# Optimization experiments

Measured on AMD Instinct MI355X. Metric: run time of the kernel, lower is better.

The kernel has to match this reference:

```python
import jax, jax.numpy as jnp
import numpy as np

PAD_IND = 3
SOS_IND = 0
NSTEPS = 25
H = 256   # hidden_size
D = 256   # input_size (embedding dim)
L = 3     # lstm_layers


def _lstm_cell(x, h, c, Wih, Whh, bih, bhh):
    # torch LSTM gate order: i, f, g, o
    g = x @ Wih.T + bih + h @ Whh.T + bhh
    i, f, gg, o = jnp.split(g, 4, axis=-1)
    c2 = jax.nn.sigmoid(f) * c + jax.nn.sigmoid(i) * jnp.tanh(gg)
    h2 = jax.nn.sigmoid(o) * jnp.tanh(c2)
    return h2, c2


def setup_inputs() -> dict:
    key = jax.random.key(0)
    ks = jax.random.split(key, 24)
    B, T = 64, 256
    Vin, C = 32000, 32000
    s = 1.0 / np.sqrt(H)

    def u(k, shape):
        return jax.random.uniform(k, shape, jnp.float32, -s, s)

    return dict(
        x=jax.random.randint(ks[0], (B, T), 0, Vin),
        target_val=jax.random.randint(ks[1], (B, NSTEPS), 0, C),
        enc_embed=jax.random.normal(ks[2], (Vin, D), jnp.float32),
        enc_Wih=u(ks[3], (L, 4 * H, D)),
        enc_Whh=u(ks[4], (L, 4 * H, H)),
        enc_bih=u(ks[5], (L, 4 * H)),
        enc_bhh=u(ks[6], (L, 4 * H)),
        Wq=u(ks[7], (H, H)), bq=u(ks[8], (H,)),
        Wk=u(ks[9], (H, H)), bk=u(ks[10], (H,)),
        Wv=u(ks[11], (H, H)), bv=u(ks[12], (H,)),
        Wo=u(ks[13], (H, H)), bo=u(ks[14], (H,)),
        dec_embed=jax.random.normal(ks[15], (C, D), jnp.float32),
        dec_Wih0=u(ks[16], (4 * H, 2 * H)),            # decoder layer 0 input is [emb; ctx] = 2H
        dec_Wih_rest=u(ks[17], (L - 1, 4 * H, H)),
        dec_Whh=u(ks[18], (L, 4 * H, H)),
        dec_bih=u(ks[19], (L, 4 * H)),
        dec_bhh=u(ks[20], (L, 4 * H)),
        dec_W=u(ks[21], (C, H)),
        dec_b=u(ks[22], (C,)),
    )


def reference(x, target_val, enc_embed, enc_Wih, enc_Whh, enc_bih, enc_bhh,
              Wq, bq, Wk, bk, Wv, bv, Wo, bo,
              dec_embed, dec_Wih0, dec_Wih_rest, dec_Whh, dec_bih, dec_bhh,
              dec_W, dec_b):
    B, T = x.shape
    lengths = (x != PAD_IND).sum(axis=1)            # [B], emulates pack_padded_sequence
    emb = enc_embed[x]                              # [B,T,D]
    valid = (jnp.arange(T)[:, None] < lengths[None, :])[..., None]  # [T,B,1]
    h0 = jnp.zeros((L, B, H), emb.dtype)
    c0 = jnp.zeros((L, B, H), emb.dtype)

    def enc_step(carry, inp):
        h, c = carry
        xt, v = inp
        hs, cs = [], []
        z = xt
        for l in range(L):
            hl, cl = _lstm_cell(z, h[l], c[l], enc_Wih[l], enc_Whh[l], enc_bih[l], enc_bhh[l])
            hl = jnp.where(v, hl, h[l])             # freeze state past sequence length
            cl = jnp.where(v, cl, c[l])
            hs.append(hl); cs.append(cl)
            z = hl
        h = jnp.stack(hs); c = jnp.stack(cs)
        return (h, c), jnp.where(v, h[-1], 0.0)     # pad_packed pads with zeros

    (enc_h, enc_c), outs = jax.lax.scan(enc_step, (h0, c0), (jnp.swapaxes(emb, 0, 1), valid))
    enc_hiddens = jnp.swapaxes(outs, 0, 1)          # [B,T,H]

    # attention key/value projections are loop-invariant -> hoist out of decode loop
    kp = enc_hiddens @ Wk.T + bk                    # [B,T,H]
    vp = enc_hiddens @ Wv.T + bv                    # [B,T,H]
    scale = 1.0 / jnp.sqrt(jnp.asarray(H, emb.dtype))
    dec_Wih = [dec_Wih0, dec_Wih_rest[0], dec_Wih_rest[1]]
    tok0 = jnp.full((B,), SOS_IND, jnp.int32)

    def dec_step(carry, _):
        h, c, tok = carry
        e = dec_embed[tok]                          # [B,D]
        q = h.sum(axis=0) @ Wq.T + bq               # prev_state[0].sum(axis=0) -> [B,H]
        scores = jnp.einsum('bh,bth->bt', q, kp) * scale
        attn = jax.nn.softmax(scores, axis=-1)
        ctx = jnp.einsum('bt,bth->bh', attn, vp) @ Wo.T + bo
        z = jnp.concatenate([e, ctx], axis=-1)      # [B,2H]
        hs, cs = [], []
        for l in range(L):
            hl, cl = _lstm_cell(z, h[l], c[l], dec_Wih[l], dec_Whh[l], dec_bih[l], dec_bhh[l])
            hs.append(hl); cs.append(cl)
            z = hl
        h = jnp.stack(hs); c = jnp.stack(cs)
        logits = z @ dec_W.T + dec_b                # [B,C]
        tok = jnp.argmax(logits, axis=-1).astype(jnp.int32)  # greedy feedback (TF ratio = 0)
        return (h, c, tok), logits

    _, logits = jax.lax.scan(dec_step, (enc_h, enc_c, tok0), None, length=NSTEPS)  # [25,B,C]
    return jnp.swapaxes(logits, 0, 1)[:, :, None, :]  # [B,25,1,C] like the torch module
```

## Files before the change

kernel.cpp:

```cpp
#include <hip/hip_runtime.h>
#include <math.h>

#define TT    256
#define NB    64
#define HH    256
#define NSTEP 25
#define NCLS  32000
#define PADI  3
#define RING  4

__device__ __align__(16) float g_hring[3][RING][NB][HH];
__device__ __align__(16) float g_enchid[TT][NB][HH];
__device__ __align__(16) float g_kp[NB][TT][HH];
__device__ __align__(16) float g_vp[NB][TT][HH];
__device__ __align__(16) float g_cfin[3][NB][HH];
__device__ __align__(16) float g_hdec[2][3][NB][HH];
__device__ __align__(16) float g_z0[NB][512];
__device__ float    g_wmax[256][NB];
__device__ int      g_wmaxi[256][NB];
__device__ int      g_len[NB];
__device__ unsigned g_arrive[256];
__device__ unsigned g_rel[256];
__device__ unsigned g_earr[3][64];
__device__ unsigned g_erel[3][64];

__device__ __forceinline__ float sigf(float v){ return 1.0f / (1.0f + expf(-v)); }

#define SCOPE_AG __HIP_MEMORY_SCOPE_AGENT
typedef unsigned long long u64;
__device__ __forceinline__ float2 ld2(const float* p){
  u64 v = __hip_atomic_load((const u64*)p, __ATOMIC_RELAXED, SCOPE_AG);
  float2 r; __builtin_memcpy(&r, &v, 8); return r;
}
__device__ __forceinline__ float ldc(const float* p){ return __hip_atomic_load(p, __ATOMIC_RELAXED, SCOPE_AG); }
__device__ __forceinline__ void  stc(float* p, float v){ __hip_atomic_store(p, v, __ATOMIC_RELAXED, SCOPE_AG); }
__device__ __forceinline__ int   ldi(const int* p){ return __hip_atomic_load(p, __ATOMIC_RELAXED, SCOPE_AG); }
__device__ __forceinline__ void  sti(int* p, int v){ __hip_atomic_store(p, v, __ATOMIC_RELAXED, SCOPE_AG); }
__device__ __forceinline__ unsigned ldu(const unsigned* p){ return __hip_atomic_load(p, __ATOMIC_RELAXED, SCOPE_AG); }
__device__ __forceinline__ void  stu(unsigned* p, unsigned v){ __hip_atomic_store(p, v, __ATOMIC_RELAXED, SCOPE_AG); }

#define DOT4(a_, x_, w_) (a_) += (x_).x*(w_).x + (x_).y*(w_).y + (x_).z*(w_).z + (x_).w*(w_).w

__global__ void __launch_bounds__(256) k_init(const int* __restrict__ p_x){
  const int blk = blockIdx.x, tid = threadIdx.x;
  if (blk < 192){
    int idx = blk*256 + tid;
    int l = idx >> 14, rem = idx & 16383;
    g_hring[l][RING-1][rem >> 8][rem & 255] = 0.f;
  } else {
    __shared__ int s_c[4];
    int b = blk - 192;
    int cnt = (p_x[b*TT + tid] != PADI) ? 1 : 0;
    #pragma unroll
    for (int m = 1; m < 64; m <<= 1) cnt += __shfl_xor(cnt, m);
    if ((tid & 63) == 0) s_c[tid >> 6] = cnt;
    __syncthreads();
    if (tid == 0) g_len[b] = s_c[0] + s_c[1] + s_c[2] + s_c[3];
  }
  if (blk == 0){ g_arrive[tid] = 0u; g_rel[tid] = 0u; }
  if (blk == 1 && tid < 192){
    ((unsigned*)g_earr)[tid] = 0u;
    ((unsigned*)g_erel)[tid] = 0u;
  }
}

__global__ void __launch_bounds__(512, 1)
k_enc(const int*   __restrict__ p_x,
      const float* __restrict__ p_eemb,
      const float* __restrict__ p_eWih, const float* __restrict__ p_eWhh,
      const float* __restrict__ p_ebih, const float* __restrict__ p_ebhh)
{
  __shared__ __align__(16) float s_W[8192];
  __shared__ float s_gat[1024];
  __shared__ float s_b[16];
  __shared__ int   s_len[64];

  const int w = blockIdx.x, tid = threadIdx.x;
  const int l = w >> 6, q = w & 63;
  const int b2 = tid >> 4, j = tid & 15;
  const int ce = tid >> 6, cb = tid & 63;

  for (int fi = tid; fi < 8192; fi += 512){
    int row = fi >> 9, k = fi & 511;
    int e = row >> 2, g = row & 3;
    int wrow = g*256 + 4*q + e;
    s_W[fi] = (k < 256) ? p_eWih[((size_t)l*1024 + wrow)*256 + k]
                        : p_eWhh[((size_t)l*1024 + wrow)*256 + (k - 256)];
  }
  if (tid < 16){
    int e = tid >> 2, g = tid & 3;
    int wrow = g*256 + 4*q + e;
    s_b[tid] = p_ebih[l*1024 + wrow] + p_ebhh[l*1024 + wrow];
  }
  if (tid < 64) s_len[tid] = g_len[tid];
  float c_reg = 0.f, h_frz = 0.f;
  __syncthreads();

  for (int t = 0; t < TT; ++t){
    if (tid == 0){
      const int li = (q & 3) << 4;
      for (;;){
        bool ok = (ldu(&g_erel[l][li]) >= (unsigned)t);
        if (ok && l > 0)          ok = (ldu(&g_erel[l-1][li]) >= (unsigned)(t+1));
        if (ok && l < 2 && t >= 4) ok = (ldu(&g_erel[l+1][li]) >= (unsigned)(t-3));
        if (ok) break;
        __builtin_amdgcn_s_sleep(1);
      }
    }
    __syncthreads();

    float4 xin[2][4], hin[2][4];
    #pragma unroll
    for (int bb = 0; bb < 2; ++bb){
      const int batch = 2*b2 + bb;
      if (l == 0){
        const float* xs = p_eemb + (size_t)p_x[batch*TT + t]*HH;
        #pragma unroll
        for (int u = 0; u < 4; ++u) xin[bb][u] = *(const float4*)(xs + u*64 + 4*j);
      } else {
        const float* xs = &g_hring[l-1][t & (RING-1)][batch][0];
        #pragma unroll
        for (int u = 0; u < 4; ++u){
          float2 a = ld2(xs + u*64 + 4*j), c = ld2(xs + u*64 + 4*j + 2);
          xin[bb][u] = make_float4(a.x, a.y, c.x, c.y);
        }
      }
      const float* hs = &g_hring[l][(t + RING - 1) & (RING-1)][batch][0];
      #pragma unroll
      for (int u = 0; u < 4; ++u){
        float2 a = ld2(hs + u*64 + 4*j), c = ld2(hs + u*64 + 4*j + 2);
        hin[bb][u] = make_float4(a.x, a.y, c.x, c.y);
      }
    }

    float acc[16][2];
    #pragma unroll
    for (int r = 0; r < 16; ++r){ acc[r][0] = 0.f; acc[r][1] = 0.f; }
    #pragma unroll
    for (int u = 0; u < 8; ++u){
      float4 i0 = (u < 4) ? xin[0][u] : hin[0][u-4];
      float4 i1 = (u < 4) ? xin[1][u] : hin[1][u-4];
      #pragma unroll
      for (int row = 0; row < 16; ++row){
        float4 wv = *(const float4*)&s_W[row*512 + u*64 + 4*j];
        DOT4(acc[row][0], i0, wv);
        DOT4(acc[row][1], i1, wv);
      }
    }
    #pragma unroll
    for (int row = 0; row < 16; ++row){
      #pragma unroll
      for (int bb = 0; bb < 2; ++bb){
        float v = acc[row][bb];
        v += __shfl_xor(v, 1); v += __shfl_xor(v, 2);
        v += __shfl_xor(v, 4); v += __shfl_xor(v, 8);
        acc[row][bb] = v;
      }
    }
    if (j == 0){
      #pragma unroll
      for (int row = 0; row < 16; ++row){
        s_gat[row*64 + 2*b2    ] = acc[row][0];
        s_gat[row*64 + 2*b2 + 1] = acc[row][1];
      }
    }
    __syncthreads();

    if (tid < 256){
      float iv = s_gat[(ce*4+0)*64 + cb] + s_b[ce*4+0];
      float fv = s_gat[(ce*4+1)*64 + cb] + s_b[ce*4+1];
      float gv = s_gat[(ce*4+2)*64 + cb] + s_b[ce*4+2];
      float ov = s_gat[(ce*4+3)*64 + cb] + s_b[ce*4+3];
      float c2 = sigf(fv)*c_reg + sigf(iv)*tanhf(gv);
      float h2 = sigf(ov)*tanhf(c2);
      bool valid = (t < s_len[cb]);
      if (valid) c_reg = c2;
      h_frz = valid ? h2 : h_frz;
      stc(&g_hring[l][t & (RING-1)][cb][4*q + ce], h_frz);
      if (l == 2) g_enchid[t][cb][4*q + ce] = valid ? h_frz : 0.f;
    }

    asm volatile("s_waitcnt vmcnt(0)" ::: "memory");
    __syncthreads();
    if (tid == 0) stu(&g_earr[l][q], (unsigned)(t+1));
    if (q == 0 && tid < 64){
      while (!__all(ldu(&g_earr[l][tid]) >= (unsigned)(t+1)))
        __builtin_amdgcn_s_sleep(1);
      if (tid < 4) stu(&g_erel[l][tid << 4], (unsigned)(t+1));
    }
    __syncthreads();
  }

  if (tid < 256) g_cfin[l][cb][4*q + ce] = c_reg;
}

__device__ __forceinline__ void gbar(int w, unsigned target){
  asm volatile("s_waitcnt vmcnt(0)" ::: "memory");
  __syncthreads();
  if (threadIdx.x == 0) stu(&g_arrive[w], target);
  if (w == 0){
    if (threadIdx.x < 64){
      const int i4 = threadIdx.x * 4;
      for (;;){
        unsigned a0 = ldu(&g_arrive[i4+0]);
        unsigned a1 = ldu(&g_arrive[i4+1]);
        unsigned a2 = ldu(&g_arrive[i4+2]);
        unsigned a3 = ldu(&g_arrive[i4+3]);
        if (__all((a0>=target) && (a1>=target) && (a2>=target) && (a3>=target))) break;
        __builtin_amdgcn_s_sleep(1);
      }
      if (threadIdx.x < 16) stu(&g_rel[threadIdx.x << 4], target);
    }
  } else {
    if (threadIdx.x == 0){
      const unsigned* line = &g_rel[(w >> 4) << 4];
      while (ldu(line) < target) __builtin_amdgcn_s_sleep(1);
    }
  }
  __syncthreads();
}

template<int NCB, int BASE>
__device__ __forceinline__ void dec_gates(const float* sw, const float* i0, const float* i1,
                                          const float* i2, int j, float out4[4]){
  float a0=0.f, a1=0.f, a2=0.f, a3=0.f;
  const float* ips[3] = { i0, i1, i2 };
  #pragma unroll
  for (int cb = 0; cb < NCB; ++cb){
    float2 xin[16];
    #pragma unroll
    for (int u = 0; u < 16; ++u) xin[u] = ld2(ips[cb] + u*16 + 2*j);
    #pragma unroll
    for (int u2 = 0; u2 < 8; ++u2){
      float2 pa = xin[2*u2], pb = xin[2*u2+1];
      const float* wb = &sw[BASE + (((cb*4+0)*8+j)*36) + u2*4];
      float4 w0 = *(const float4*)(wb);
      float4 w1 = *(const float4*)(wb + 288);
      float4 w2 = *(const float4*)(wb + 576);
      float4 w3 = *(const float4*)(wb + 864);
      a0 += pa.x*w0.x + pa.y*w0.y + pb.x*w0.z + pb.y*w0.w;
      a1 += pa.x*w1.x + pa.y*w1.y + pb.x*w1.z + pb.y*w1.w;
      a2 += pa.x*w2.x + pa.y*w2.y + pb.x*w2.z + pb.y*w2.w;
      a3 += pa.x*w3.x + pa.y*w3.y + pb.x*w3.z + pb.y*w3.w;
    }
  }
  #pragma unroll
  for (int m = 1; m < 8; m <<= 1){
    a0 += __shfl_xor(a0, m); a1 += __shfl_xor(a1, m);
    a2 += __shfl_xor(a2, m); a3 += __shfl_xor(a3, m);
  }
  out4[0]=a0; out4[1]=a1; out4[2]=a2; out4[3]=a3;
}

__global__ void __launch_bounds__(512, 1)
k_dec(const float* __restrict__ p_Wq, const float* __restrict__ p_bq,
      const float* __restrict__ p_Wk, const float* __restrict__ p_bk,
      const float* __restrict__ p_Wv, const float* __restrict__ p_bv,
      const float* __restrict__ p_Wo, const float* __restrict__ p_bo,
      const float* __restrict__ p_demb,
      const float* __restrict__ p_dWih0, const float* __restrict__ p_dWihR,
      const float* __restrict__ p_dWhh,
      const float* __restrict__ p_dbih,  const float* __restrict__ p_dbhh,
      const float* __restrict__ p_dW,    const float* __restrict__ p_db,
      float* __restrict__ p_out)
{
  __shared__ __align__(16) float s_w[8064];
  __shared__ __align__(16) float s_h2[NB*HH];
  __shared__ float s_bdec[12];
  __shared__ __align__(16) float s_hs[256];
  __shared__ __align__(16) float s_q[256];
  __shared__ __align__(16) float s_sc[256];
  __shared__ __align__(16) float s_at[256];
  __shared__ __align__(16) float s_ctx[256];
  __shared__ float s_rv[8];  __shared__ int s_ri[8];

  const int w   = blockIdx.x;
  const int tid = threadIdx.x;
  const int b   = tid >> 3;
  const int j   = tid & 7;
  unsigned bar  = 0;

  {
    const int b3 = w >> 2, t0 = (w & 3) * 64;
    const int n1 = tid & 127, rq = tid >> 7;
    for (int p = 0; p < 4; ++p){
      const int n = p*128 + n1;
      const float* wrow = (n < 256) ? (p_Wk + (size_t)n*HH) : (p_Wv + (size_t)(n-256)*HH);
      const float bias  = (n < 256) ? p_bk[n] : p_bv[n-256];
      const float4* wr4 = (const float4*)wrow;
      const float* hb = &g_enchid[t0 + rq*16][b3][0];
      const float4* hr[16];
      #pragma unroll
      for (int r = 0; r < 16; ++r) hr[r] = (const float4*)(hb + (size_t)r*NB*HH);
      float a16[16];
      #pragma unroll
      for (int r = 0; r < 16; ++r) a16[r] = 0.f;
      for (int k4 = 0; k4 < 64; ++k4){
        float4 wv = wr4[k4];
        #pragma unroll
        for (int r = 0; r < 16; ++r){ float4 h4 = hr[r][k4]; DOT4(a16[r], h4, wv); }
      }
      float* orow = (n < 256) ? &g_kp[b3][t0 + rq*16][n] : &g_vp[b3][t0 + rq*16][n-256];
      #pragma unroll
      for (int r = 0; r < 16; ++r) stc(orow + (size_t)r*HH, a16[r] + bias);
    }
  }

  for (int fi = tid; fi < 3072; fi += 512){
    int g = fi / 768, k = fi % 768; int row = g*256 + w;
    float v = (k < 512) ? p_dWih0[(size_t)row*512 + k]
                        : p_dWhh[(size_t)row*HH + (k - 512)];
    int cb = k >> 8, kk = k & 255;
    s_w[(((cb*4 + g)*8 + ((kk & 15) >> 1))*36) + (((kk >> 4) << 1) | (kk & 1))] = v;
  }
  for (int fi = tid; fi < 2048; fi += 512){
    int g = fi / 512, k = fi % 512; int row = g*256 + w;
    float v = (k < 256) ? p_dWihR[(size_t)row*HH + k]
                        : p_dWhh[(size_t)(1024 + row)*HH + (k - 256)];
    int cb = k >> 8, kk = k & 255;
    s_w[3456 + (((cb*4 + g)*8 + ((kk & 15) >> 1))*36) + (((kk >> 4) << 1) | (kk & 1))] = v;
  }
  for (int fi = tid; fi < 2048; fi += 512){
    int g = fi / 512, k = fi % 512; int row = g*256 + w;
    float v = (k < 256) ? p_dWihR[(size_t)(1024 + row)*HH + k]
                        : p_dWhh[(size_t)(2048 + row)*HH + (k - 256)];
    int cb = k >> 8, kk = k & 255;
    s_w[5760 + (((cb*4 + g)*8 + ((kk & 15) >> 1))*36) + (((kk >> 4) << 1) | (kk & 1))] = v;
  }
  if (tid < 12){
    int l = tid >> 2, g = tid & 3; int row = g*256 + w;
    s_bdec[tid] = p_dbih[l*1024 + row] + p_dbhh[l*1024 + row];
  }
  gbar(w, ++bar);

  if (tid < 192){
    int fi = w*192 + tid;
    int l = fi >> 14, rem = fi & 16383;
    stc(&g_hdec[0][l][rem >> 8][rem & 255], ldc(&g_hring[l][RING-1][rem >> 8][rem & 255]));
  }
  float c_d0 = 0.f, c_d1 = 0.f, c_d2 = 0.f;
  if (j == 0){
    c_d0 = g_cfin[0][b][w]; c_d1 = g_cfin[1][b][w]; c_d2 = g_cfin[2][b][w];
  }
  gbar(w, ++bar);

  for (int st = 0; st < NSTEP; ++st){
    const int slot = st & 1, nxt = slot ^ 1;

    if (w < 64){
      const int bA = w;
      int tok = 0;
      if (st > 0){
        float v = -1e38f; int idx = 0;
        if (tid < 256){ v = ldc(&g_wmax[tid][bA]); idx = ldi(&g_wmaxi[tid][bA]); }
        #pragma unroll
        for (int m = 1; m < 64; m <<= 1){
          float ov = __shfl_xor(v, m); int oi = __shfl_xor(idx, m);
          if (ov > v || (ov == v && oi < idx)){ v = ov; idx = oi; }
        }
        if ((tid & 63) == 0){ s_rv[tid >> 6] = v; s_ri[tid >> 6] = idx; }
        __syncthreads();
        if (tid == 0){
          float bv2 = s_rv[0]; int bi2 = s_ri[0];
          for (int q2 = 1; q2 < 8; ++q2){
            float ov = s_rv[q2]; int oi = s_ri[q2];
            if (ov > bv2 || (ov == bv2 && oi < bi2)){ bv2 = ov; bi2 = oi; }
          }
          s_ri[0] = bi2;
        }
        __syncthreads();
        tok = s_ri[0];
      }
      if (tid < 256)
        s_hs[tid] = ldc(&g_hdec[slot][0][bA][tid]) + ldc(&g_hdec[slot][1][bA][tid])
                  + ldc(&g_hdec[slot][2][bA][tid]);
      __syncthreads();
      if (tid < 256){
        float a = p_bq[tid];
        const float4* wr = (const float4*)(p_Wq + (size_t)tid*HH);
        #pragma unroll 8
        for (int k4 = 0; k4 < 64; ++k4){
          float4 wv = wr[k4]; float4 h4 = *(const float4*)&s_hs[k4*4]; DOT4(a, h4, wv);
        }
        s_q[tid] = a;
      }
      __syncthreads();
      if (tid < 256){
        float a = 0.f;
        const float4* kr = (const float4*)&g_kp[bA][tid][0];
        #pragma unroll 8
        for (int k4 = 0; k4 < 64; ++k4){
          float4 kv = kr[k4]; float4 q4 = *(const float4*)&s_q[k4*4]; DOT4(a, q4, kv);
        }
        s_sc[tid] = a * 0.0625f;
      }
      __syncthreads();
      {
        float sv = (tid < 256) ? s_sc[tid] : -1e38f;
        float m2 = sv;
        #pragma unroll
        for (int m = 1; m < 64; m <<= 1) m2 = fmaxf(m2, __shfl_xor(m2, m));
        if ((tid & 63) == 0) s_rv[tid >> 6] = m2;
        __syncthreads();
        if (tid == 0){ float mm = s_rv[0]; for (int q2 = 1; q2 < 8; ++q2) mm = fmaxf(mm, s_rv[q2]); s_rv[0] = mm; }
        __syncthreads();
        const float mx = s_rv[0];
        float ev = (tid < 256) ? expf(sv - mx) : 0.f;
        float ss = ev;
        #pragma unroll
        for (int m = 1; m < 64; m <<= 1) ss += __shfl_xor(ss, m);
        __syncthreads();
        if ((tid & 63) == 0) s_rv[tid >> 6] = ss;
        __syncthreads();
        if (tid == 0){ float t2 = 0.f; for (int q2 = 0; q2 < 8; ++q2) t2 += s_rv[q2]; s_rv[0] = t2; }
        __syncthreads();
        if (tid < 256) s_at[tid] = ev / s_rv[0];
      }
      __syncthreads();
      if (tid < 256){
        float a = 0.f;
        const float* vb = &g_vp[bA][0][tid];
        #pragma unroll 4
        for (int t4 = 0; t4 < 64; ++t4){
          float4 a4 = *(const float4*)&s_at[t4*4];
          a += a4.x*vb[(size_t)(t4*4+0)*HH] + a4.y*vb[(size_t)(t4*4+1)*HH]
             + a4.z*vb[(size_t)(t4*4+2)*HH] + a4.w*vb[(size_t)(t4*4+3)*HH];
        }
        s_ctx[tid] = a;
      }
      __syncthreads();
      if (tid < 256){
        float a = p_bo[tid];
        const float4* wr = (const float4*)(p_Wo + (size_t)tid*HH);
        #pragma unroll 8
        for (int k4 = 0; k4 < 64; ++k4){
          float4 wv = wr[k4]; float4 c4 = *(const float4*)&s_ctx[k4*4]; DOT4(a, c4, wv);
        }
        stc(&g_z0[bA][256 + tid], a);
        stc(&g_z0[bA][tid], p_demb[(size_t)tok*HH + tid]);
      }
    }
    gbar(w, ++bar);

    {
      float g4[4];
      dec_gates<3, 0>(s_w, &g_z0[b][0], &g_z0[b][256], &g_hdec[slot][0][b][0], j, g4);
      if (j == 0){
        float iv = g4[0]+s_bdec[0], fv = g4[1]+s_bdec[1], gv = g4[2]+s_bdec[2], ov = g4[3]+s_bdec[3];
        float c2 = sigf(fv)*c_d0 + sigf(iv)*tanhf(gv); c_d0 = c2;
        stc(&g_hdec[nxt][0][b][w], sigf(ov)*tanhf(c2));
      }
    }
    gbar(w, ++bar);
    {
      float g4[4];
      dec_gates<2, 3456>(s_w, &g_hdec[nxt][0][b][0], &g_hdec[slot][1][b][0], nullptr, j, g4);
      if (j == 0){
        float iv = g4[0]+s_bdec[4], fv = g4[1]+s_bdec[5], gv = g4[2]+s_bdec[6], ov = g4[3]+s_bdec[7];
        float c2 = sigf(fv)*c_d1 + sigf(iv)*tanhf(gv); c_d1 = c2;
        stc(&g_hdec[nxt][1][b][w], sigf(ov)*tanhf(c2));
      }
    }
    gbar(w, ++bar);
    {
      float g4[4];
      dec_gates<2, 5760>(s_w, &g_hdec[nxt][1][b][0], &g_hdec[slot][2][b][0], nullptr, j, g4);
      if (j == 0){
        float iv = g4[0]+s_bdec[8], fv = g4[1]+s_bdec[9], gv = g4[2]+s_bdec[10], ov = g4[3]+s_bdec[11];
        float c2 = sigf(fv)*c_d2 + sigf(iv)*tanhf(gv); c_d2 = c2;
        stc(&g_hdec[nxt][2][b][w], sigf(ov)*tanhf(c2));
      }
    }
    gbar(w, ++bar);

    {
      {
        const float* src = &g_hdec[nxt][2][0][0];
        #pragma unroll
        for (int u = 0; u < 16; ++u){
          int fo = 2*(tid + 512*u);
          float2 v = ld2(src + fo);
          *(float2*)(s_h2 + fo) = v;
        }
      }
      __syncthreads();

      const int cs = tid & 63, qb = tid >> 6;
      const bool ok0 = (2*cs)   < 125;
      const bool ok1 = (2*cs+1) < 125;
      const int c0 = w*125 + 2*cs, c1 = c0 + 1;
      const float4* wr0 = (const float4*)(p_dW + (size_t)(ok0 ? c0 : w*125)*HH);
      const float4* wr1 = (const float4*)(p_dW + (size_t)(ok1 ? c1 : w*125)*HH);
      const float4* zr[8];
      #pragma unroll
      for (int r = 0; r < 8; ++r) zr[r] = (const float4*)&s_h2[(qb*8 + r)*HH];
      float a0[8], a1[8];
      #pragma unroll
      for (int r = 0; r < 8; ++r){ a0[r] = 0.f; a1[r] = 0.f; }
      for (int k4 = 0; k4 < 64; ++k4){
        float4 w0 = wr0[k4], w1 = wr1[k4];
        #pragma unroll
        for (int r = 0; r < 8; ++r){
          float4 z4 = zr[r][k4];
          DOT4(a0[r], z4, w0);
          DOT4(a1[r], z4, w1);
        }
      }
      const float bias0 = ok0 ? p_db[c0] : 0.f;
      const float bias1 = ok1 ? p_db[c1] : 0.f;
      #pragma unroll
      for (int r = 0; r < 8; ++r){
        const int bb = qb*8 + r;
        float val0 = a0[r] + bias0, val1 = a1[r] + bias1;
        float* orow = p_out + ((size_t)bb*NSTEP + st)*NCLS;
        if (ok0) orow[c0] = val0;
        if (ok1) orow[c1] = val1;
        float v = ok0 ? val0 : -1e38f;
        int idx  = ok0 ? c0 : 0x7fffffff;
        if (ok1 && val1 > v){ v = val1; idx = c1; }
        #pragma unroll
        for (int m = 1; m < 64; m <<= 1){
          float ov = __shfl_xor(v, m); int oi = __shfl_xor(idx, m);
          if (ov > v || (ov == v && oi < idx)){ v = ov; idx = oi; }
        }
        if (cs == 0){ stc(&g_wmax[w][bb], v); sti(&g_wmaxi[w][bb], idx); }
      }
    }
    gbar(w, ++bar);
  }
}

extern "C" void kernel_launch(void* const* d_in, const int* in_sizes, int n_in,
                              void* d_out, int out_size, void* d_ws, size_t ws_size,
                              hipStream_t stream){
  (void)in_sizes; (void)n_in; (void)out_size; (void)d_ws; (void)ws_size;
  const int*   x     = (const int*)d_in[0];
  const float* eemb  = (const float*)d_in[2];
  const float* eWih  = (const float*)d_in[3];
  const float* eWhh  = (const float*)d_in[4];
  const float* ebih  = (const float*)d_in[5];
  const float* ebhh  = (const float*)d_in[6];
  const float* Wq    = (const float*)d_in[7];
  const float* bq    = (const float*)d_in[8];
  const float* Wk    = (const float*)d_in[9];
  const float* bk    = (const float*)d_in[10];
  const float* Wv    = (const float*)d_in[11];
  const float* bv    = (const float*)d_in[12];
  const float* Wo    = (const float*)d_in[13];
  const float* bo    = (const float*)d_in[14];
  const float* demb  = (const float*)d_in[15];
  const float* dWih0 = (const float*)d_in[16];
  const float* dWihR = (const float*)d_in[17];
  const float* dWhh  = (const float*)d_in[18];
  const float* dbih  = (const float*)d_in[19];
  const float* dbhh  = (const float*)d_in[20];
  const float* dW    = (const float*)d_in[21];
  const float* db    = (const float*)d_in[22];
  float* out = (float*)d_out;

  k_init<<<dim3(256), dim3(256), 0, stream>>>(x);
  k_enc<<<dim3(192), dim3(512), 0, stream>>>(x, eemb, eWih, eWhh, ebih, ebhh);
  k_dec<<<dim3(256), dim3(512), 0, stream>>>(Wq, bq, Wk, bk, Wv, bv, Wo, bo,
                                             demb, dWih0, dWihR, dWhh, dbih, dbhh,
                                             dW, db, out);
}
```

Measured before the change: 5.717 ms.

## Split persistent decoder into per-step kernel launches and retile encoder dot products

Replaces the persistent decoder kernel and its software grid barriers with a sequence of small kernels per decode step (attention, three LSTM layers, output projection), using kernel boundaries as synchronization and keeping cell state in global memory. The encoder matvec is also retiled so each thread group covers 4 batches with 32-lane reductions instead of 2 batches with 16-lane reductions. This removes spin-barrier overhead but adds about 125 kernel launches plus reloading decoder weights into shared memory every step.

After: 7.895 ms. +38.1%, slower.

```diff
diff --git a/kernel.cpp b/kernel.cpp
--- a/kernel.cpp
+++ b/kernel.cpp
@@ -15,12 +15,11 @@
 __device__ __align__(16) float g_vp[NB][TT][HH];
 __device__ __align__(16) float g_cfin[3][NB][HH];
 __device__ __align__(16) float g_hdec[2][3][NB][HH];
+__device__ __align__(16) float g_cdec[3][NB][HH];
 __device__ __align__(16) float g_z0[NB][512];
 __device__ float    g_wmax[256][NB];
 __device__ int      g_wmaxi[256][NB];
 __device__ int      g_len[NB];
-__device__ unsigned g_arrive[256];
-__device__ unsigned g_rel[256];
 __device__ unsigned g_earr[3][64];
 __device__ unsigned g_erel[3][64];
 
@@ -32,10 +31,7 @@
   u64 v = __hip_atomic_load((const u64*)p, __ATOMIC_RELAXED, SCOPE_AG);
   float2 r; __builtin_memcpy(&r, &v, 8); return r;
 }
-__device__ __forceinline__ float ldc(const float* p){ return __hip_atomic_load(p, __ATOMIC_RELAXED, SCOPE_AG); }
 __device__ __forceinline__ void  stc(float* p, float v){ __hip_atomic_store(p, v, __ATOMIC_RELAXED, SCOPE_AG); }
-__device__ __forceinline__ int   ldi(const int* p){ return __hip_atomic_load(p, __ATOMIC_RELAXED, SCOPE_AG); }
-__device__ __forceinline__ void  sti(int* p, int v){ __hip_atomic_store(p, v, __ATOMIC_RELAXED, SCOPE_AG); }
 __device__ __forceinline__ unsigned ldu(const unsigned* p){ return __hip_atomic_load(p, __ATOMIC_RELAXED, SCOPE_AG); }
 __device__ __forceinline__ void  stu(unsigned* p, unsigned v){ __hip_atomic_store(p, v, __ATOMIC_RELAXED, SCOPE_AG); }
 
@@ -57,8 +53,7 @@
     __syncthreads();
     if (tid == 0) g_len[b] = s_c[0] + s_c[1] + s_c[2] + s_c[3];
   }
-  if (blk == 0){ g_arrive[tid] = 0u; g_rel[tid] = 0u; }
-  if (blk == 1 && tid < 192){
+  if (blk == 0 && tid < 192){
     ((unsigned*)g_earr)[tid] = 0u;
     ((unsigned*)g_erel)[tid] = 0u;
   }
@@ -77,8 +72,8 @@
 
   const int w = blockIdx.x, tid = threadIdx.x;
   const int l = w >> 6, q = w & 63;
-  const int b2 = tid >> 4, j = tid & 15;
-  const int ce = tid >> 6, cb = tid & 63;
+  const int bg = tid >> 5, j = tid & 31;
+  const int cb = (tid & 255) >> 2, ce = tid & 3;
 
   for (int fi = tid; fi < 8192; fi += 512){
     int row = fi >> 9, k = fi & 511;
@@ -96,72 +91,64 @@
   float c_reg = 0.f, h_frz = 0.f;
   __syncthreads();
 
+  const int li = (q & 3) << 4;
   for (int t = 0; t < TT; ++t){
     if (tid == 0){
-      const int li = (q & 3) << 4;
       for (;;){
         bool ok = (ldu(&g_erel[l][li]) >= (unsigned)t);
-        if (ok && l > 0)          ok = (ldu(&g_erel[l-1][li]) >= (unsigned)(t+1));
-        if (ok && l < 2 && t >= 4) ok = (ldu(&g_erel[l+1][li]) >= (unsigned)(t-3));
+        if (ok && l > 0)               ok = (ldu(&g_erel[l-1][li]) >= (unsigned)(t+1));
+        if (ok && l < 2 && t >= RING)  ok = (ldu(&g_erel[l+1][li]) >= (unsigned)(t-(RING-1)));
         if (ok) break;
         __builtin_amdgcn_s_sleep(1);
       }
     }
     __syncthreads();
 
-    float4 xin[2][4], hin[2][4];
-    #pragma unroll
-    for (int bb = 0; bb < 2; ++bb){
-      const int batch = 2*b2 + bb;
+    float4 xin[4][4];
+    #pragma unroll
+    for (int bb = 0; bb < 4; ++bb){
+      const int batch = 4*bg + bb;
       if (l == 0){
         const float* xs = p_eemb + (size_t)p_x[batch*TT + t]*HH;
-        #pragma unroll
-        for (int u = 0; u < 4; ++u) xin[bb][u] = *(const float4*)(xs + u*64 + 4*j);
+        xin[bb][0] = *(const float4*)(xs + 4*j);
+        xin[bb][1] = *(const float4*)(xs + 128 + 4*j);
       } else {
         const float* xs = &g_hring[l-1][t & (RING-1)][batch][0];
+        { float2 a = ld2(xs + 4*j),       c2 = ld2(xs + 4*j + 2);       xin[bb][0] = make_float4(a.x,a.y,c2.x,c2.y); }
+        { float2 a = ld2(xs + 128 + 4*j), c2 = ld2(xs + 128 + 4*j + 2); xin[bb][1] = make_float4(a.x,a.y,c2.x,c2.y); }
+      }
+      const float* hs = &g_hring[l][(t + RING - 1) & (RING-1)][batch][0];
+      { float2 a = ld2(hs + 4*j),       c2 = ld2(hs + 4*j + 2);       xin[bb][2] = make_float4(a.x,a.y,c2.x,c2.y); }
+      { float2 a = ld2(hs + 128 + 4*j), c2 = ld2(hs + 128 + 4*j + 2); xin[bb][3] = make_float4(a.x,a.y,c2.x,c2.y); }
+    }
+
+    float acc[16][4];
+    #pragma unroll
+    for (int r = 0; r < 16; ++r){ acc[r][0]=0.f; acc[r][1]=0.f; acc[r][2]=0.f; acc[r][3]=0.f; }
+    #pragma unroll
+    for (int c = 0; c < 4; ++c){
+      #pragma unroll
+      for (int r = 0; r < 16; ++r){
+        float4 wv = *(const float4*)&s_W[r*512 + c*128 + 4*j];
         #pragma unroll
-        for (int u = 0; u < 4; ++u){
-          float2 a = ld2(xs + u*64 + 4*j), c = ld2(xs + u*64 + 4*j + 2);
-          xin[bb][u] = make_float4(a.x, a.y, c.x, c.y);
-        }
-      }
-      const float* hs = &g_hring[l][(t + RING - 1) & (RING-1)][batch][0];
+        for (int bb = 0; bb < 4; ++bb) DOT4(acc[r][bb], xin[bb][c], wv);
+      }
+    }
+    #pragma unroll
+    for (int r = 0; r < 16; ++r){
       #pragma unroll
-      for (int u = 0; u < 4; ++u){
-        float2 a = ld2(hs + u*64 + 4*j), c = ld2(hs + u*64 + 4*j + 2);
-        hin[bb][u] = make_float4(a.x, a.y, c.x, c.y);
-      }
-    }
-
-    float acc[16][2];
-    #pragma unroll
-    for (int r = 0; r < 16; ++r){ acc[r][0] = 0.f; acc[r][1] = 0.f; }
-    #pragma unroll
-    for (int u = 0; u < 8; ++u){
-      float4 i0 = (u < 4) ? xin[0][u] : hin[0][u-4];
-      float4 i1 = (u < 4) ? xin[1][u] : hin[1][u-4];
-      #pragma unroll
-      for (int row = 0; row < 16; ++row){
-        float4 wv = *(const float4*)&s_W[row*512 + u*64 + 4*j];
-        DOT4(acc[row][0], i0, wv);
-        DOT4(acc[row][1], i1, wv);
-      }
-    }
-    #pragma unroll
-    for (int row = 0; row < 16; ++row){
-      #pragma unroll
-      for (int bb = 0; bb < 2; ++bb){
-        float v = acc[row][bb];
-        v += __shfl_xor(v, 1); v += __shfl_xor(v, 2);
-        v += __shfl_xor(v, 4); v += __shfl_xor(v, 8);
-        acc[row][bb] = v;
+      for (int bb = 0; bb < 4; ++bb){
+        float v = acc[r][bb];
+        v += __shfl_xor(v,1); v += __shfl_xor(v,2); v += __shfl_xor(v,4);
+        v += __shfl_xor(v,8); v += __shfl_xor(v,16);
+        acc[r][bb] = v;
       }
     }
     if (j == 0){
       #pragma unroll
-      for (int row = 0; row < 16; ++row){
-        s_gat[row*64 + 2*b2    ] = acc[row][0];
-        s_gat[row*64 + 2*b2 + 1] = acc[row][1];
+      for (int r = 0; r < 16; ++r){
+        #pragma unroll
+        for (int bb = 0; bb < 4; ++bb) s_gat[r*64 + 4*bg + bb] = acc[r][bb];
       }
     }
     __syncthreads();
@@ -190,96 +177,14 @@
     }
     __syncthreads();
   }
-
   if (tid < 256) g_cfin[l][cb][4*q + ce] = c_reg;
 }
 
-__device__ __forceinline__ void gbar(int w, unsigned target){
-  asm volatile("s_waitcnt vmcnt(0)" ::: "memory");
-  __syncthreads();
-  if (threadIdx.x == 0) stu(&g_arrive[w], target);
-  if (w == 0){
-    if (threadIdx.x < 64){
-      const int i4 = threadIdx.x * 4;
-      for (;;){
-        unsigned a0 = ldu(&g_arrive[i4+0]);
-        unsigned a1 = ldu(&g_arrive[i4+1]);
-        unsigned a2 = ldu(&g_arrive[i4+2]);
-        unsigned a3 = ldu(&g_arrive[i4+3]);
-        if (__all((a0>=target) && (a1>=target) && (a2>=target) && (a3>=target))) break;
-        __builtin_amdgcn_s_sleep(1);
-      }
-      if (threadIdx.x < 16) stu(&g_rel[threadIdx.x << 4], target);
-    }
-  } else {
-    if (threadIdx.x == 0){
-      const unsigned* line = &g_rel[(w >> 4) << 4];
-      while (ldu(line) < target) __builtin_amdgcn_s_sleep(1);
-    }
-  }
-  __syncthreads();
-}
-
-template<int NCB, int BASE>
-__device__ __forceinline__ void dec_gates(const float* sw, const float* i0, const float* i1,
-                                          const float* i2, int j, float out4[4]){
-  float a0=0.f, a1=0.f, a2=0.f, a3=0.f;
-  const float* ips[3] = { i0, i1, i2 };
-  #pragma unroll
-  for (int cb = 0; cb < NCB; ++cb){
-    float2 xin[16];
-    #pragma unroll
-    for (int u = 0; u < 16; ++u) xin[u] = ld2(ips[cb] + u*16 + 2*j);
-    #pragma unroll
-    for (int u2 = 0; u2 < 8; ++u2){
-      float2 pa = xin[2*u2], pb = xin[2*u2+1];
-      const float* wb = &sw[BASE + (((cb*4+0)*8+j)*36) + u2*4];
-      float4 w0 = *(const float4*)(wb);
-      float4 w1 = *(const float4*)(wb + 288);
-      float4 w2 = *(const float4*)(wb + 576);
-      float4 w3 = *(const float4*)(wb + 864);
-      a0 += pa.x*w0.x + pa.y*w0.y + pb.x*w0.z + pb.y*w0.w;
-      a1 += pa.x*w1.x + pa.y*w1.y + pb.x*w1.z + pb.y*w1.w;
-      a2 += pa.x*w2.x + pa.y*w2.y + pb.x*w2.z + pb.y*w2.w;
-      a3 += pa.x*w3.x + pa.y*w3.y + pb.x*w3.z + pb.y*w3.w;
-    }
-  }
-  #pragma unroll
-  for (int m = 1; m < 8; m <<= 1){
-    a0 += __shfl_xor(a0, m); a1 += __shfl_xor(a1, m);
-    a2 += __shfl_xor(a2, m); a3 += __shfl_xor(a3, m);
-  }
-  out4[0]=a0; out4[1]=a1; out4[2]=a2; out4[3]=a3;
-}
-
-__global__ void __launch_bounds__(512, 1)
-k_dec(const float* __restrict__ p_Wq, const float* __restrict__ p_bq,
-      const float* __restrict__ p_Wk, const float* __restrict__ p_bk,
-      const float* __restrict__ p_Wv, const float* __restrict__ p_bv,
-      const float* __restrict__ p_Wo, const float* __restrict__ p_bo,
-      const float* __restrict__ p_demb,
-      const float* __restrict__ p_dWih0, const float* __restrict__ p_dWihR,
-      const float* __restrict__ p_dWhh,
-      const float* __restrict__ p_dbih,  const float* __restrict__ p_dbhh,
-      const float* __restrict__ p_dW,    const float* __restrict__ p_db,
-      float* __restrict__ p_out)
-{
-  __shared__ __align__(16) float s_w[8064];
-  __shared__ __align__(16) float s_h2[NB*HH];
-  __shared__ float s_bdec[12];
-  __shared__ __align__(16) float s_hs[256];
-  __shared__ __align__(16) float s_q[256];
-  __shared__ __align__(16) float s_sc[256];
-  __shared__ __align__(16) float s_at[256];
-  __shared__ __align__(16) float s_ctx[256];
-  __shared__ float s_rv[8];  __shared__ int s_ri[8];
-
-  const int w   = blockIdx.x;
-  const int tid = threadIdx.x;
-  const int b   = tid >> 3;
-  const int j   = tid & 7;
-  unsigned bar  = 0;
-
+__global__ void __launch_bounds__(512)
+k_kv(const float* __restrict__ p_Wk, const float* __restrict__ p_bk,
+     const float* __restrict__ p_Wv, const float* __restrict__ p_bv)
+{
+  const int w = blockIdx.x, tid = threadIdx.x;
   {
     const int b3 = w >> 2, t0 = (w & 3) * 64;
     const int n1 = tid & 127, rq = tid >> 7;
@@ -302,10 +207,162 @@
       }
       float* orow = (n < 256) ? &g_kp[b3][t0 + rq*16][n] : &g_vp[b3][t0 + rq*16][n-256];
       #pragma unroll
-      for (int r = 0; r < 16; ++r) stc(orow + (size_t)r*HH, a16[r] + bias);
-    }
-  }
-
+      for (int r = 0; r < 16; ++r) orow[(size_t)r*HH] = a16[r] + bias;
+    }
+  }
+  const int gidx = w*512 + tid;
+  if (gidx < 49152){
+    ((float*)g_cdec)[gidx] = ((const float*)g_cfin)[gidx];
+    int l = gidx >> 14, rem = gidx & 16383;
+    ((float*)g_hdec)[gidx] = g_hring[l][RING-1][rem >> 8][rem & 255];
+  }
+}
+
+__global__ void __launch_bounds__(256)
+k_a(int st,
+    const float* __restrict__ p_Wq, const float* __restrict__ p_bq,
+    const float* __restrict__ p_Wo, const float* __restrict__ p_bo,
+    const float* __restrict__ p_demb)
+{
+  __shared__ __align__(16) float s_hs[256];
+  __shared__ __align__(16) float s_q[256];
+  __shared__ __align__(16) float s_sc[256];
+  __shared__ __align__(16) float s_at[256];
+  __shared__ __align__(16) float s_ctx[256];
+  __shared__ float s_rv[4]; __shared__ int s_ri[4];
+
+  const int bA = blockIdx.x, tid = threadIdx.x;
+  const int slot = st & 1;
+  int tok = 0;
+  if (st > 0){
+    float v = g_wmax[tid][bA]; int idx = g_wmaxi[tid][bA];
+    #pragma unroll
+    for (int m = 1; m < 64; m <<= 1){
+      float ov = __shfl_xor(v, m); int oi = __shfl_xor(idx, m);
+      if (ov > v || (ov == v && oi < idx)){ v = ov; idx = oi; }
+    }
+    if ((tid & 63) == 0){ s_rv[tid >> 6] = v; s_ri[tid >> 6] = idx; }
+    __syncthreads();
+    if (tid == 0){
+      float bv = s_rv[0]; int bi = s_ri[0];
+      for (int q2 = 1; q2 < 4; ++q2){
+        float ov = s_rv[q2]; int oi = s_ri[q2];
+        if (ov > bv || (ov == bv && oi < bi)){ bv = ov; bi = oi; }
+      }
+      s_ri[0] = bi;
+    }
+    __syncthreads();
+    tok = s_ri[0];
+  }
+  s_hs[tid] = g_hdec[slot][0][bA][tid] + g_hdec[slot][1][bA][tid] + g_hdec[slot][2][bA][tid];
+  __syncthreads();
+  {
+    float a = p_bq[tid];
+    const float4* wr = (const float4*)(p_Wq + (size_t)tid*HH);
+    #pragma unroll 8
+    for (int k4 = 0; k4 < 64; ++k4){
+      float4 wv = wr[k4]; float4 h4 = *(const float4*)&s_hs[k4*4]; DOT4(a, h4, wv);
+    }
+    s_q[tid] = a;
+  }
+  __syncthreads();
+  {
+    float a = 0.f;
+    const float4* kr = (const float4*)&g_kp[bA][tid][0];
+    #pragma unroll 8
+    for (int k4 = 0; k4 < 64; ++k4){
+      float4 kv = kr[k4]; float4 q4 = *(const float4*)&s_q[k4*4]; DOT4(a, q4, kv);
+    }
+    s_sc[tid] = a * 0.0625f;
+  }
+  __syncthreads();
+  {
+    float sv = s_sc[tid];
+    float m2 = sv;
+    #pragma unroll
+    for (int m = 1; m < 64; m <<= 1) m2 = fmaxf(m2, __shfl_xor(m2, m));
+    if ((tid & 63) == 0) s_rv[tid >> 6] = m2;
+    __syncthreads();
+    if (tid == 0){ float mm = s_rv[0]; for (int q2 = 1; q2 < 4; ++q2) mm = fmaxf(mm, s_rv[q2]); s_rv[0] = mm; }
+    __syncthreads();
+    const float mx = s_rv[0];
+    float ev = expf(sv - mx);
+    float ss = ev;
+    #pragma unroll
+    for (int m = 1; m < 64; m <<= 1) ss += __shfl_xor(ss, m);
+    __syncthreads();
+    if ((tid & 63) == 0) s_rv[tid >> 6] = ss;
+    __syncthreads();
+    if (tid == 0){ float t2 = 0.f; for (int q2 = 0; q2 < 4; ++q2) t2 += s_rv[q2]; s_rv[0] = t2; }
+    __syncthreads();
+    s_at[tid] = ev / s_rv[0];
+  }
+  __syncthreads();
+  {
+    float a = 0.f;
+    const float* vb = &g_vp[bA][0][tid];
+    #pragma unroll 4
+    for (int t4 = 0; t4 < 64; ++t4){
+      float4 a4 = *(const float4*)&s_at[t4*4];
+      a += a4.x*vb[(size_t)(t4*4+0)*HH] + a4.y*vb[(size_t)(t4*4+1)*HH]
+         + a4.z*vb[(size_t)(t4*4+2)*HH] + a4.w*vb[(size_t)(t4*4+3)*HH];
+    }
+    s_ctx[tid] = a;
+  }
+  __syncthreads();
+  {
+    float a = p_bo[tid];
+    const float4* wr = (const float4*)(p_Wo + (size_t)tid*HH);
+    #pragma unroll 8
+    for (int k4 = 0; k4 < 64; ++k4){
+      float4 wv = wr[k4]; float4 c4 = *(const float4*)&s_ctx[k4*4]; DOT4(a, c4, wv);
+    }
+    g_z0[bA][256 + tid] = a;
+    g_z0[bA][tid] = p_demb[(size_t)tok*HH + tid];
+  }
+}
+
+template<int NCB>
+__device__ __forceinline__ void dec_gates_p(const float* sw, const float* i0, const float* i1,
+                                            const float* i2, int j, float out4[4]){
+  float a0=0.f, a1=0.f, a2=0.f, a3=0.f;
+  const float* ips[3] = { i0, i1, i2 };
+  #pragma unroll
+  for (int cb = 0; cb < NCB; ++cb){
+    float2 xin[16];
+    #pragma unroll
+    for (int u = 0; u < 16; ++u) xin[u] = *(const float2*)(ips[cb] + u*16 + 2*j);
+    #pragma unroll
+    for (int u2 = 0; u2 < 8; ++u2){
+      float2 pa = xin[2*u2], pb = xin[2*u2+1];
+      const float* wb = &sw[(((cb*4+0)*8+j)*36) + u2*4];
+      float4 w0 = *(const float4*)(wb);
+      float4 w1 = *(const float4*)(wb + 288);
+      float4 w2 = *(const float4*)(wb + 576);
+      float4 w3 = *(const float4*)(wb + 864);
+      a0 += pa.x*w0.x + pa.y*w0.y + pb.x*w0.z + pb.y*w0.w;
+      a1 += pa.x*w1.x + pa.y*w1.y + pb.x*w1.z + pb.y*w1.w;
+      a2 += pa.x*w2.x + pa.y*w2.y + pb.x*w2.z + pb.y*w2.w;
+      a3 += pa.x*w3.x + pa.y*w3.y + pb.x*w3.z + pb.y*w3.w;
+    }
+  }
+  #pragma unroll
+  for (int m = 1; m < 8; m <<= 1){
+    a0 += __shfl_xor(a0, m); a1 += __shfl_xor(a1, m);
+    a2 += __shfl_xor(a2, m); a3 += __shfl_xor(a3, m);
+  }
+  out4[0]=a0; out4[1]=a1; out4[2]=a2; out4[3]=a3;
+}
+
+__global__ void __launch_bounds__(512)
+k_b(int st, const float* __restrict__ p_dWih0, const float* __restrict__ p_dWhh,
+    const float* __restrict__ p_dbih, const float* __restrict__ p_dbhh)
+{
+  __shared__ __align__(16) float s_w[3456];
+  __shared__ float s_bd[4];
+  const int w = blockIdx.x, tid = threadIdx.x;
+  const int b = tid >> 3, j = tid & 7;
+  const int slot = st & 1, nxt = slot ^ 1;
   for (int fi = tid; fi < 3072; fi += 512){
     int g = fi / 768, k = fi % 768; int row = g*256 + w;
     float v = (k < 512) ? p_dWih0[(size_t)row*512 + k]
@@ -313,220 +370,128 @@
     int cb = k >> 8, kk = k & 255;
     s_w[(((cb*4 + g)*8 + ((kk & 15) >> 1))*36) + (((kk >> 4) << 1) | (kk & 1))] = v;
   }
+  if (tid < 4) s_bd[tid] = p_dbih[tid*256 + w] + p_dbhh[tid*256 + w];
+  __syncthreads();
+  float g4[4];
+  dec_gates_p<3>(s_w, &g_z0[b][0], &g_z0[b][256], &g_hdec[slot][0][b][0], j, g4);
+  if (j == 0){
+    float iv=g4[0]+s_bd[0], fv=g4[1]+s_bd[1], gv=g4[2]+s_bd[2], ov=g4[3]+s_bd[3];
+    float c2 = sigf(fv)*g_cdec[0][b][w] + sigf(iv)*tanhf(gv);
+    g_cdec[0][b][w] = c2;
+    g_hdec[nxt][0][b][w] = sigf(ov)*tanhf(c2);
+  }
+}
+
+__global__ void __launch_bounds__(512)
+k_c(int st, const float* __restrict__ p_dWihR, const float* __restrict__ p_dWhh,
+    const float* __restrict__ p_dbih, const float* __restrict__ p_dbhh)
+{
+  __shared__ __align__(16) float s_w[2304];
+  __shared__ float s_bd[4];
+  const int w = blockIdx.x, tid = threadIdx.x;
+  const int b = tid >> 3, j = tid & 7;
+  const int slot = st & 1, nxt = slot ^ 1;
   for (int fi = tid; fi < 2048; fi += 512){
     int g = fi / 512, k = fi % 512; int row = g*256 + w;
     float v = (k < 256) ? p_dWihR[(size_t)row*HH + k]
                         : p_dWhh[(size_t)(1024 + row)*HH + (k - 256)];
     int cb = k >> 8, kk = k & 255;
-    s_w[3456 + (((cb*4 + g)*8 + ((kk & 15) >> 1))*36) + (((kk >> 4) << 1) | (kk & 1))] = v;
-  }
+    s_w[(((cb*4 + g)*8 + ((kk & 15) >> 1))*36) + (((kk >> 4) << 1) | (kk & 1))] = v;
+  }
+  if (tid < 4) s_bd[tid] = p_dbih[1024 + tid*256 + w] + p_dbhh[1024 + tid*256 + w];
+  __syncthreads();
+  float g4[4];
+  dec_gates_p<2>(s_w, &g_hdec[nxt][0][b][0], &g_hdec[slot][1][b][0], nullptr, j, g4);
+  if (j == 0){
+    float iv=g4[0]+s_bd[0], fv=g4[1]+s_bd[1], gv=g4[2]+s_bd[2], ov=g4[3]+s_bd[3];
+    float c2 = sigf(fv)*g_cdec[1][b][w] + sigf(iv)*tanhf(gv);
+    g_cdec[1][b][w] = c2;
+    g_hdec[nxt][1][b][w] = sigf(ov)*tanhf(c2);
+  }
+}
+
+__global__ void __launch_bounds__(512)
+k_d(int st, const float* __restrict__ p_dWihR, const float* __restrict__ p_dWhh,
+    const float* __restrict__ p_dbih, const float* __restrict__ p_dbhh)
+{
+  __shared__ __align__(16) float s_w[2304];
+  __shared__ float s_bd[4];
+  const int w = blockIdx.x, tid = threadIdx.x;
+  const int b = tid >> 3, j = tid & 7;
+  const int slot = st & 1, nxt = slot ^ 1;
   for (int fi = tid; fi < 2048; fi += 512){
     int g = fi / 512, k = fi % 512; int row = g*256 + w;
     float v = (k < 256) ? p_dWihR[(size_t)(1024 + row)*HH + k]
                         : p_dWhh[(size_t)(2048 + row)*HH + (k - 256)];
     int cb = k >> 8, kk = k & 255;
-    s_w[5760 + (((cb*4 + g)*8 + ((kk & 15) >> 1))*36) + (((kk >> 4) << 1) | (kk & 1))] = v;
-  }
-  if (tid < 12){
-    int l = tid >> 2, g = tid & 3; int row = g*256 + w;
-    s_bdec[tid] = p_dbih[l*1024 + row] + p_dbhh[l*1024 + row];
-  }
-  gbar(w, ++bar);
-
-  if (tid < 192){
-    int fi = w*192 + tid;
-    int l = fi >> 14, rem = fi & 16383;
-    stc(&g_hdec[0][l][rem >> 8][rem & 255], ldc(&g_hring[l][RING-1][rem >> 8][rem & 255]));
-  }
-  float c_d0 = 0.f, c_d1 = 0.f, c_d2 = 0.f;
+    s_w[(((cb*4 + g)*8 + ((kk & 15) >> 1))*36) + (((kk >> 4) << 1) | (kk & 1))] = v;
+  }
+  if (tid < 4) s_bd[tid] = p_dbih[2048 + tid*256 + w] + p_dbhh[2048 + tid*256 + w];
+  __syncthreads();
+  float g4[4];
+  dec_gates_p<2>(s_w, &g_hdec[nxt][1][b][0], &g_hdec[slot][2][b][0], nullptr, j, g4);
   if (j == 0){
-    c_d0 = g_cfin[0][b][w]; c_d1 = g_cfin[1][b][w]; c_d2 = g_cfin[2][b][w];
-  }
-  gbar(w, ++bar);
-
-  for (int st = 0; st < NSTEP; ++st){
-    const int slot = st & 1, nxt = slot ^ 1;
-
-    if (w < 64){
-      const int bA = w;
-      int tok = 0;
-      if (st > 0){
-        float v = -1e38f; int idx = 0;
-        if (tid < 256){ v = ldc(&g_wmax[tid][bA]); idx = ldi(&g_wmaxi[tid][bA]); }
-        #pragma unroll
-        for (int m = 1; m < 64; m <<= 1){
-          float ov = __shfl_xor(v, m); int oi = __shfl_xor(idx, m);
-          if (ov > v || (ov == v && oi < idx)){ v = ov; idx = oi; }
-        }
-        if ((tid & 63) == 0){ s_rv[tid >> 6] = v; s_ri[tid >> 6] = idx; }
-        __syncthreads();
-        if (tid == 0){
-          float bv2 = s_rv[0]; int bi2 = s_ri[0];
-          for (int q2 = 1; q2 < 8; ++q2){
-            float ov = s_rv[q2]; int oi = s_ri[q2];
-            if (ov > bv2 || (ov == bv2 && oi < bi2)){ bv2 = ov; bi2 = oi; }
-          }
-          s_ri[0] = bi2;
-        }
-        __syncthreads();
-        tok = s_ri[0];
-      }
-      if (tid < 256)
-        s_hs[tid] = ldc(&g_hdec[slot][0][bA][tid]) + ldc(&g_hdec[slot][1][bA][tid])
-                  + ldc(&g_hdec[slot][2][bA][tid]);
-      __syncthreads();
-      if (tid < 256){
-        float a = p_bq[tid];
-        const float4* wr = (const float4*)(p_Wq + (size_t)tid*HH);
-        #pragma unroll 8
-        for (int k4 = 0; k4 < 64; ++k4){
-          float4 wv = wr[k4]; float4 h4 = *(const float4*)&s_hs[k4*4]; DOT4(a, h4, wv);
-        }
-        s_q[tid] = a;
-      }
-      __syncthreads();
-      if (tid < 256){
-        float a = 0.f;
-        const float4* kr = (const float4*)&g_kp[bA][tid][0];
-        #pragma unroll 8
-        for (int k4 = 0; k4 < 64; ++k4){
-          float4 kv = kr[k4]; float4 q4 = *(const float4*)&s_q[k4*4]; DOT4(a, q4, kv);
-        }
-        s_sc[tid] = a * 0.0625f;
-      }
-      __syncthreads();
-      {
-        float sv = (tid < 256) ? s_sc[tid] : -1e38f;
-        float m2 = sv;
-        #pragma unroll
-        for (int m = 1; m < 64; m <<= 1) m2 = fmaxf(m2, __shfl_xor(m2, m));
-        if ((tid & 63) == 0) s_rv[tid >> 6] = m2;
-        __syncthreads();
-        if (tid == 0){ float mm = s_rv[0]; for (int q2 = 1; q2 < 8; ++q2) mm = fmaxf(mm, s_rv[q2]); s_rv[0] = mm; }
-        __syncthreads();
-        const float mx = s_rv[0];
-        float ev = (tid < 256) ? expf(sv - mx) : 0.f;
-        float ss = ev;
-        #pragma unroll
-        for (int m = 1; m < 64; m <<= 1) ss += __shfl_xor(ss, m);
-        __syncthreads();
-        if ((tid & 63) == 0) s_rv[tid >> 6] = ss;
-        __syncthreads();
-        if (tid == 0){ float t2 = 0.f; for (int q2 = 0; q2 < 8; ++q2) t2 += s_rv[q2]; s_rv[0] = t2; }
-        __syncthreads();
-        if (tid < 256) s_at[tid] = ev / s_rv[0];
-      }
-      __syncthreads();
-      if (tid < 256){
-        float a = 0.f;
-        const float* vb = &g_vp[bA][0][tid];
-        #pragma unroll 4
-        for (int t4 = 0; t4 < 64; ++t4){
-          float4 a4 = *(const float4*)&s_at[t4*4];
-          a += a4.x*vb[(size_t)(t4*4+0)*HH] + a4.y*vb[(size_t)(t4*4+1)*HH]
-             + a4.z*vb[(size_t)(t4*4+2)*HH] + a4.w*vb[(size_t)(t4*4+3)*HH];
-        }
-        s_ctx[tid] = a;
-      }
-      __syncthreads();
-      if (tid < 256){
-        float a = p_bo[tid];
-        const float4* wr = (const float4*)(p_Wo + (size_t)tid*HH);
-        #pragma unroll 8
-        for (int k4 = 0; k4 < 64; ++k4){
-          float4 wv = wr[k4]; float4 c4 = *(const float4*)&s_ctx[k4*4]; DOT4(a, c4, wv);
-        }
-        stc(&g_z0[bA][256 + tid], a);
-        stc(&g_z0[bA][tid], p_demb[(size_t)tok*HH + tid]);
-      }
-    }
-    gbar(w, ++bar);
-
-    {
-      float g4[4];
-      dec_gates<3, 0>(s_w, &g_z0[b][0], &g_z0[b][256], &g_hdec[slot][0][b][0], j, g4);
-      if (j == 0){
-        float iv = g4[0]+s_bdec[0], fv = g4[1]+s_bdec[1], gv = g4[2]+s_bdec[2], ov = g4[3]+s_bdec[3];
-        float c2 = sigf(fv)*c_d0 + sigf(iv)*tanhf(gv); c_d0 = c2;
-        stc(&g_hdec[nxt][0][b][w], sigf(ov)*tanhf(c2));
-      }
-    }
-    gbar(w, ++bar);
-    {
-      float g4[4];
-      dec_gates<2, 3456>(s_w, &g_hdec[nxt][0][b][0], &g_hdec[slot][1][b][0], nullptr, j, g4);
-      if (j == 0){
-        float iv = g4[0]+s_bdec[4], fv = g4[1]+s_bdec[5], gv = g4[2]+s_bdec[6], ov = g4[3]+s_bdec[7];
-        float c2 = sigf(fv)*c_d1 + sigf(iv)*tanhf(gv); c_d1 = c2;
-        stc(&g_hdec[nxt][1][b][w], sigf(ov)*tanhf(c2));
-      }
-    }
-    gbar(w, ++bar);
-    {
-      float g4[4];
-      dec_gates<2, 5760>(s_w, &g_hdec[nxt][1][b][0], &g_hdec[slot][2][b][0], nullptr, j, g4);
-      if (j == 0){
-        float iv = g4[0]+s_bdec[8], fv = g4[1]+s_bdec[9], gv = g4[2]+s_bdec[10], ov = g4[3]+s_bdec[11];
-        float c2 = sigf(fv)*c_d2 + sigf(iv)*tanhf(gv); c_d2 = c2;
-        stc(&g_hdec[nxt][2][b][w], sigf(ov)*tanhf(c2));
-      }
-    }
-    gbar(w, ++bar);
-
-    {
-      {
-        const float* src = &g_hdec[nxt][2][0][0];
-        #pragma unroll
-        for (int u = 0; u < 16; ++u){
-          int fo = 2*(tid + 512*u);
-          float2 v = ld2(src + fo);
-          *(float2*)(s_h2 + fo) = v;
-        }
-      }
-      __syncthreads();
-
-      const int cs = tid & 63, qb = tid >> 6;
-      const bool ok0 = (2*cs)   < 125;
-      const bool ok1 = (2*cs+1) < 125;
-      const int c0 = w*125 + 2*cs, c1 = c0 + 1;
-      const float4* wr0 = (const float4*)(p_dW + (size_t)(ok0 ? c0 : w*125)*HH);
-      const float4* wr1 = (const float4*)(p_dW + (size_t)(ok1 ? c1 : w*125)*HH);
-      const float4* zr[8];
-      #pragma unroll
-      for (int r = 0; r < 8; ++r) zr[r] = (const float4*)&s_h2[(qb*8 + r)*HH];
-      float a0[8], a1[8];
-      #pragma unroll
-      for (int r = 0; r < 8; ++r){ a0[r] = 0.f; a1[r] = 0.f; }
-      for (int k4 = 0; k4 < 64; ++k4){
-        float4 w0 = wr0[k4], w1 = wr1[k4];
-        #pragma unroll
-        for (int r = 0; r < 8; ++r){
-          float4 z4 = zr[r][k4];
-          DOT4(a0[r], z4, w0);
-          DOT4(a1[r], z4, w1);
-        }
-      }
-      const float bias0 = ok0 ? p_db[c0] : 0.f;
-      const float bias1 = ok1 ? p_db[c1] : 0.f;
-      #pragma unroll
-      for (int r = 0; r < 8; ++r){
-        const int bb = qb*8 + r;
-        float val0 = a0[r] + bias0, val1 = a1[r] + bias1;
-        float* orow = p_out + ((size_t)bb*NSTEP + st)*NCLS;
-        if (ok0) orow[c0] = val0;
-        if (ok1) orow[c1] = val1;
-        float v = ok0 ? val0 : -1e38f;
-        int idx  = ok0 ? c0 : 0x7fffffff;
-        if (ok1 && val1 > v){ v = val1; idx = c1; }
-        #pragma unroll
-        for (int m = 1; m < 64; m <<= 1){
-          float ov = __shfl_xor(v, m); int oi = __shfl_xor(idx, m);
-          if (ov > v || (ov == v && oi < idx)){ v = ov; idx = oi; }
-        }
-        if (cs == 0){ stc(&g_wmax[w][bb], v); sti(&g_wmaxi[w][bb], idx); }
-      }
-    }
-    gbar(w, ++bar);
+    float iv=g4[0]+s_bd[0], fv=g4[1]+s_bd[1], gv=g4[2]+s_bd[2], ov=g4[3]+s_bd[3];
+    float c2 = sigf(fv)*g_cdec[2][b][w] + sigf(iv)*tanhf(gv);
+    g_cdec[2][b][w] = c2;
+    g_hdec[nxt][2][b][w] = sigf(ov)*tanhf(c2);
+  }
+}
+
+__global__ void __launch_bounds__(512)
+k_e(int st, const float* __restrict__ p_dW, const float* __restrict__ p_db,
+    float* __restrict__ p_out)
+{
+  __shared__ __align__(16) float s_h2[NB*HH];
+  const int w = blockIdx.x, tid = threadIdx.x;
+  const int nxt = (st & 1) ^ 1;
+  {
+    const float4* src = (const float4*)&g_hdec[nxt][2][0][0];
+    float4* dst = (float4*)s_h2;
+    #pragma unroll
+    for (int u = 0; u < 8; ++u){ int i4 = tid + 512*u; dst[i4] = src[i4]; }
+  }
+  __syncthreads();
+
+  const int cs = tid & 63, qb = tid >> 6;
+  const bool ok0 = (2*cs)   < 125;
+  const bool ok1 = (2*cs+1) < 125;
+  const int c0 = w*125 + 2*cs, c1 = c0 + 1;
+  const float4* wr0 = (const float4*)(p_dW + (size_t)(ok0 ? c0 : w*125)*HH);
+  const float4* wr1 = (const float4*)(p_dW + (size_t)(ok1 ? c1 : w*125)*HH);
+  const float4* zr[8];
+  #pragma unroll
+  for (int r = 0; r < 8; ++r) zr[r] = (const float4*)&s_h2[(qb*8 + r)*HH];
+  float a0[8], a1[8];
+  #pragma unroll
+  for (int r = 0; r < 8; ++r){ a0[r] = 0.f; a1[r] = 0.f; }
+  for (int k4 = 0; k4 < 64; ++k4){
+    float4 w0 = wr0[k4], w1 = wr1[k4];
+    #pragma unroll
+    for (int r = 0; r < 8; ++r){
+      float4 z4 = zr[r][k4];
+      DOT4(a0[r], z4, w0);
+      DOT4(a1[r], z4, w1);
+    }
+  }
+  const float bias0 = ok0 ? p_db[c0] : 0.f;
+  const float bias1 = ok1 ? p_db[c1] : 0.f;
+  #pragma unroll
+  for (int r = 0; r < 8; ++r){
+    const int bb = qb*8 + r;
+    float val0 = a0[r] + bias0, val1 = a1[r] + bias1;
+    float* orow = p_out + ((size_t)bb*NSTEP + st)*NCLS;
+    if (ok0) orow[c0] = val0;
+    if (ok1) orow[c1] = val1;
+    float v = ok0 ? val0 : -1e38f;
+    int idx  = ok0 ? c0 : 0x7fffffff;
+    if (ok1 && val1 > v){ v = val1; idx = c1; }
+    #pragma unroll
+    for (int m = 1; m < 64; m <<= 1){
+      float ov = __shfl_xor(v, m); int oi = __shfl_xor(idx, m);
+      if (ov > v || (ov == v && oi < idx)){ v = ov; idx = oi; }
+    }
+    if (cs == 0){ g_wmax[w][bb] = v; g_wmaxi[w][bb] = idx; }
   }
 }
 
@@ -560,7 +525,12 @@
 
   k_init<<<dim3(256), dim3(256), 0, stream>>>(x);
   k_enc<<<dim3(192), dim3(512), 0, stream>>>(x, eemb, eWih, eWhh, ebih, ebhh);
-  k_dec<<<dim3(256), dim3(512), 0, stream>>>(Wq, bq, Wk, bk, Wv, bv, Wo, bo,
-                                             demb, dWih0, dWihR, dWhh, dbih, dbhh,
-                                             dW, db, out);
-}
+  k_kv<<<dim3(256), dim3(512), 0, stream>>>(Wk, bk, Wv, bv);
+  for (int st = 0; st < NSTEP; ++st){
+    k_a<<<dim3(64),  dim3(256), 0, stream>>>(st, Wq, bq, Wo, bo, demb);
+    k_b<<<dim3(256), dim3(512), 0, stream>>>(st, dWih0, dWhh, dbih, dbhh);
+    k_c<<<dim3(256), dim3(512), 0, stream>>>(st, dWihR, dWhh, dbih, dbhh);
+    k_d<<<dim3(256), dim3(512), 0, stream>>>(st, dWihR, dWhh, dbih, dbhh);
+    k_e<<<dim3(256), dim3(512), 0, stream>>>(st, dW, db, out);
+  }
+}
```
